# Optimization experiments

Hardware: AMD Instinct MI355X
Metric: run time of the kernel (lower is better)

Reference implementation:

```python
import jax, jax.numpy as jnp
import numpy as np

L, B, S, D, H, FF, V = 4, 2, 1024, 768, 12, 3072, 50257
HD = D // H  # 64
EPS = 1e-5


def _ln(x, w, b):
    m = jnp.mean(x, axis=-1, keepdims=True)
    v = jnp.mean(jnp.square(x - m), axis=-1, keepdims=True)
    return (x - m) * jax.lax.rsqrt(v + EPS) * w + b


def setup_inputs() -> dict:
    key = jax.random.key(0)
    ks = jax.random.split(key, 8)
    std = 0.02
    inp = {
        'input_ids': jax.random.randint(ks[0], (B, S), 0, V),
        'tok_emb': jax.random.normal(ks[1], (V, D), jnp.float32) * std,
        'pos_emb': jax.random.normal(ks[2], (S, D), jnp.float32) * std,
        'ln1_w': jnp.ones((L, D), jnp.float32),
        'ln1_b': jnp.zeros((L, D), jnp.float32),
        'qkv_w': jax.random.normal(ks[3], (L, 3 * D, D), jnp.float32) * std,
        'qkv_b': jnp.zeros((L, 3 * D), jnp.float32),
        'out_w': jax.random.normal(ks[4], (L, D, D), jnp.float32) * std,
        'out_b': jnp.zeros((L, D), jnp.float32),
        'ln2_w': jnp.ones((L, D), jnp.float32),
        'ln2_b': jnp.zeros((L, D), jnp.float32),
        'fc1_w': jax.random.normal(ks[5], (L, FF, D), jnp.float32) * std,
        'fc1_b': jnp.zeros((L, FF), jnp.float32),
        'fc2_w': jax.random.normal(ks[6], (L, D, FF), jnp.float32) * std,
        'fc2_b': jnp.zeros((L, D), jnp.float32),
        'lnf_w': jnp.ones((D,), jnp.float32),
        'lnf_b': jnp.zeros((D,), jnp.float32),
    }
    return inp


def _gpt_forward(input_ids, tok_emb, pos_emb, ln1_w, ln1_b, qkv_w, qkv_b,
                 out_w, out_b, ln2_w, ln2_b, fc1_w, fc1_b, fc2_w, fc2_b,
                 lnf_w, lnf_b):
    x = tok_emb[input_ids] + pos_emb[None, :S, :]  # [B,S,D]
    causal = jnp.tril(jnp.ones((S, S), bool))  # [S,S]
    scale = 1.0 / np.sqrt(HD)
    for l in range(L):
        # --- attention ---
        h = _ln(x, ln1_w[l], ln1_b[l])
        qkv = h @ qkv_w[l].T + qkv_b[l]  # [B,S,3D]
        qkv = qkv.reshape(B, S, 3, H, HD).transpose(2, 0, 3, 1, 4)
        q, k, v = qkv[0], qkv[1], qkv[2]  # [B,H,S,HD]
        scores = jnp.einsum('bhqd,bhkd->bhqk', q, k) * scale
        scores = jnp.where(causal, scores, -jnp.inf)
        w = jax.nn.softmax(scores, axis=-1)
        a = jnp.einsum('bhqk,bhkd->bhqd', w, v)  # [B,H,S,HD]
        a = a.transpose(0, 2, 1, 3).reshape(B, S, D)
        x = x + a @ out_w[l].T + out_b[l]
        # --- ffn ---
        h = _ln(x, ln2_w[l], ln2_b[l])
        h = jax.nn.gelu(h @ fc1_w[l].T + fc1_b[l], approximate=False)
        x = x + h @ fc2_w[l].T + fc2_b[l]
    x = _ln(x, lnf_w, lnf_b)
    logits = x @ tok_emb.T  # tied lm_head, no bias
    return logits


def reference(input_ids, tok_emb, pos_emb, ln1_w, ln1_b, qkv_w, qkv_b,
              out_w, out_b, ln2_w, ln2_b, fc1_w, fc1_b, fc2_w, fc2_b,
              lnf_w, lnf_b):
    return _gpt_forward(input_ids, tok_emb, pos_emb, ln1_w, ln1_b, qkv_w,
                        qkv_b, out_w, out_b, ln2_w, ln2_b, fc1_w, fc1_b,
                        fc2_w, fc2_b, lnf_w, lnf_b)
```

## Files before the change

### kernel.cpp

```cpp
#include <hip/hip_runtime.h>
#include <cstdint>
#include <cstddef>

#define D_MODEL 768
#define NHEAD   12
#define SEQ     1024
#define NTOK    2048
#define FFDIM   3072
#define NLAYER  4
#define VOCAB   50257
#define QKVD    2304

typedef float f32x4 __attribute__((ext_vector_type(4)));
typedef __bf16 bf16x8 __attribute__((ext_vector_type(8)));

__device__ __forceinline__ unsigned short f2bf(float f) {
  unsigned int u = __float_as_uint(f);
  return (unsigned short)((u + 0x7FFFu + ((u >> 16) & 1u)) >> 16);
}

__global__ __launch_bounds__(256) void k_cvt(const float* __restrict__ in,
                                             unsigned short* __restrict__ out, int n8) {
  int i = blockIdx.x * 256 + threadIdx.x;
  if (i >= n8) return;
  const float4* p = (const float4*)in;
  float4 a = p[2 * i], b = p[2 * i + 1];
  union { unsigned short u[8]; uint4 v; } r;
  r.u[0] = f2bf(a.x); r.u[1] = f2bf(a.y); r.u[2] = f2bf(a.z); r.u[3] = f2bf(a.w);
  r.u[4] = f2bf(b.x); r.u[5] = f2bf(b.y); r.u[6] = f2bf(b.z); r.u[7] = f2bf(b.w);
  ((uint4*)out)[i] = r.v;
}

__global__ __launch_bounds__(256) void k_embed(const int* __restrict__ ids,
                                               const float* __restrict__ tok,
                                               const float* __restrict__ pos,
                                               float* __restrict__ x) {
  int gid = blockIdx.x * 256 + threadIdx.x;
  int t = gid / 192, f = gid - t * 192;
  int id = ids[t];
  float4 a = ((const float4*)tok)[(size_t)id * 192 + f];
  float4 b = ((const float4*)pos)[(size_t)(t & (SEQ - 1)) * 192 + f];
  float4 o; o.x = a.x + b.x; o.y = a.y + b.y; o.z = a.z + b.z; o.w = a.w + b.w;
  ((float4*)x)[gid] = o;
}

__global__ __launch_bounds__(256) void k_ln(const float* __restrict__ x,
                                            const float* __restrict__ w,
                                            const float* __restrict__ b,
                                            unsigned short* __restrict__ out) {
  __shared__ float red[256];
  int row = blockIdx.x, tid = threadIdx.x;
  const float* xr = x + (size_t)row * D_MODEL;
  float v0 = xr[tid], v1 = xr[tid + 256], v2 = xr[tid + 512];
  red[tid] = v0 + v1 + v2;
  __syncthreads();
  for (int o = 128; o > 0; o >>= 1) { if (tid < o) red[tid] += red[tid + o]; __syncthreads(); }
  float mean = red[0] * (1.0f / 768.0f);
  __syncthreads();
  float d0 = v0 - mean, d1 = v1 - mean, d2 = v2 - mean;
  red[tid] = d0 * d0 + d1 * d1 + d2 * d2;
  __syncthreads();
  for (int o = 128; o > 0; o >>= 1) { if (tid < o) red[tid] += red[tid + o]; __syncthreads(); }
  float rstd = rsqrtf(red[0] * (1.0f / 768.0f) + 1e-5f);
  unsigned short* orow = out + (size_t)row * D_MODEL;
  orow[tid]       = f2bf(d0 * rstd * w[tid]       + b[tid]);
  orow[tid + 256] = f2bf(d1 * rstd * w[tid + 256] + b[tid + 256]);
  orow[tid + 512] = f2bf(d2 * rstd * w[tid + 512] + b[tid + 512]);
}

__global__ __launch_bounds__(64) void k_attn(const unsigned short* __restrict__ qkv,
                                             unsigned short* __restrict__ attO) {
  int bid = blockIdx.x;
  int qt = (SEQ / 16 - 1) - (bid & 63);
  int h = (bid >> 6) % NHEAD;
  int b = bid / (64 * NHEAD);
  int lane = threadIdx.x;
  int fr = lane & 15, fq = lane >> 4;
  int qb = qt * 16;

  size_t rowQ = (size_t)(b * SEQ + qb + fr) * QKVD + h * 64;
  bf16x8 bq0 = *(const bf16x8*)(qkv + rowQ + fq * 8);
  bf16x8 bq1 = *(const bf16x8*)(qkv + rowQ + 32 + fq * 8);

  float m = -1e30f, ll = 0.0f;
  f32x4 o[4] = {};
  int nkt = (qt >> 1) + 1;
  size_t kvrow0 = (size_t)(b * SEQ) * QKVD;

  for (int kt = 0; kt < nkt; ++kt) {
    int kvb = kt * 32;
    bool diag = (kt == nkt - 1);
    float p[2][4];
    float tm = -1e30f;
    #pragma unroll
    for (int t = 0; t < 2; ++t) {
      size_t rowK = kvrow0 + (size_t)(kvb + t * 16 + fr) * QKVD + D_MODEL + h * 64;
      bf16x8 ak0 = *(const bf16x8*)(qkv + rowK + fq * 8);
      bf16x8 ak1 = *(const bf16x8*)(qkv + rowK + 32 + fq * 8);
      f32x4 st = {};
      st = __builtin_amdgcn_mfma_f32_16x16x32_bf16(ak0, bq0, st, 0, 0, 0);
      st = __builtin_amdgcn_mfma_f32_16x16x32_bf16(ak1, bq1, st, 0, 0, 0);
      #pragma unroll
      for (int j = 0; j < 4; ++j) {
        float s = st[j] * 0.125f;
        if (diag && (kvb + t * 16 + fq * 4 + j > qb + fr)) s = -1e30f;
        p[t][j] = s;
        tm = fmaxf(tm, s);
      }
    }
    tm = fmaxf(tm, __shfl_xor(tm, 16));
    tm = fmaxf(tm, __shfl_xor(tm, 32));
    float mnew = fmaxf(m, tm);
    float corr = __expf(m - mnew);
    float psum = 0.0f;
    #pragma unroll
    for (int t = 0; t < 2; ++t)
      #pragma unroll
      for (int j = 0; j < 4; ++j) { float e = __expf(p[t][j] - mnew); p[t][j] = e; psum += e; }
    psum += __shfl_xor(psum, 16);
    psum += __shfl_xor(psum, 32);
    ll = ll * corr + psum;
    m = mnew;
    #pragma unroll
    for (int dg = 0; dg < 4; ++dg) {
      o[dg][0] *= corr; o[dg][1] *= corr; o[dg][2] *= corr; o[dg][3] *= corr;
    }
    unsigned int lo0 = (unsigned)f2bf(p[0][0]) | ((unsigned)f2bf(p[0][1]) << 16);
    unsigned int hi0 = (unsigned)f2bf(p[0][2]) | ((unsigned)f2bf(p[0][3]) << 16);
    unsigned int lo1 = (unsigned)f2bf(p[1][0]) | ((unsigned)f2bf(p[1][1]) << 16);
    unsigned int hi1 = (unsigned)f2bf(p[1][2]) | ((unsigned)f2bf(p[1][3]) << 16);
    int sA = fr + 16 * ((fq & 1) * 2);
    int sB = sA + 16;
    unsigned int w0a = __shfl(lo0, sA), w0b = __shfl(lo1, sA);
    unsigned int w1a = __shfl(hi0, sA), w1b = __shfl(hi1, sA);
    unsigned int w2a = __shfl(lo0, sB), w2b = __shfl(lo1, sB);
    unsigned int w3a = __shfl(hi0, sB), w3b = __shfl(hi1, sB);
    bool t1 = (fq >> 1) != 0;
    uint4 pw;
    pw.x = t1 ? w0b : w0a;
    pw.y = t1 ? w1b : w1a;
    pw.z = t1 ? w2b : w2a;
    pw.w = t1 ? w3b : w3a;
    bf16x8 pb = __builtin_bit_cast(bf16x8, pw);
    size_t vcol = kvrow0 + 2 * D_MODEL + h * 64 + fr;
    #pragma unroll
    for (int dg = 0; dg < 4; ++dg) {
      union { unsigned short u[8]; bf16x8 v; } va;
      #pragma unroll
      for (int j = 0; j < 8; ++j)
        va.u[j] = qkv[vcol + (size_t)(kvb + fq * 8 + j) * QKVD + dg * 16];
      o[dg] = __builtin_amdgcn_mfma_f32_16x16x32_bf16(va.v, pb, o[dg], 0, 0, 0);
    }
  }
  float inv = 1.0f / ll;
  size_t obase = (size_t)(b * SEQ + qb + fr) * D_MODEL + h * 64;
  #pragma unroll
  for (int dg = 0; dg < 4; ++dg)
    #pragma unroll
    for (int j = 0; j < 4; ++j)
      attO[obase + dg * 16 + fq * 4 + j] = f2bf(o[dg][j] * inv);
}

template<int HAS_BIAS, int DO_GELU, int HAS_RES, int OUT_BF16>
__global__ __launch_bounds__(256) void k_gemm(const unsigned short* __restrict__ A,
                                              const unsigned short* __restrict__ W,
                                              const float* __restrict__ bias,
                                              const float* __restrict__ res,
                                              void* __restrict__ Cout,
                                              int N, int K) {
  __shared__ __align__(1024) unsigned short As[128 * 64];
  __shared__ __align__(1024) unsigned short Ws[128 * 64];
  int tid = threadIdx.x, lane = tid & 63, wv = tid >> 6;
  int fr = lane & 15, fq = lane >> 4;
  int wm = wv >> 1, wn = wv & 1;

  int cpx = gridDim.x >> 3;
  int id = (blockIdx.x & 7) * cpx + (blockIdx.x >> 3);
  int bm = (id & 15) * 128;
  int bn = (id >> 4) * 128;

  const unsigned short* pA[4];
  const unsigned short* pW[4];
  unsigned short* ldsA[4];
  unsigned short* ldsW[4];
  #pragma unroll
  for (int i = 0; i < 4; ++i) {
    int c = wv * 4 + i;
    int r = c * 8 + (lane >> 3);
    int up = (lane & 7) ^ (r & 7);
    pA[i] = A + (size_t)(bm + r) * K + up * 8;
    int wr = bn + r; if (wr > N - 1) wr = N - 1;
    pW[i] = W + (size_t)wr * K + up * 8;
    ldsA[i] = &As[c * 512];
    ldsW[i] = &Ws[c * 512];
  }

  const unsigned short* aB = As + (wm * 64 + fr) * 64;
  const unsigned short* wB = Ws + (wn * 64 + fr) * 64;
  int sz = fr & 7;
  int u0 = (fq ^ sz) * 8;
  int u1 = ((4 + fq) ^ sz) * 8;

  f32x4 acc[4][4] = {};

  for (int k0 = 0; k0 < K; k0 += 64) {
    #pragma unroll
    for (int i = 0; i < 4; ++i) {
      __builtin_amdgcn_global_load_lds(
          (const __attribute__((address_space(1))) unsigned int*)(pA[i] + k0),
          (__attribute__((address_space(3))) unsigned int*)ldsA[i], 16, 0, 0);
      __builtin_amdgcn_global_load_lds(
          (const __attribute__((address_space(1))) unsigned int*)(pW[i] + k0),
          (__attribute__((address_space(3))) unsigned int*)ldsW[i], 16, 0, 0);
    }
    __syncthreads();

    bf16x8 af[4][2], bf[4][2];
    #pragma unroll
    for (int mm = 0; mm < 4; ++mm) {
      af[mm][0] = *(const bf16x8*)(aB + mm * 1024 + u0);
      af[mm][1] = *(const bf16x8*)(aB + mm * 1024 + u1);
    }
    #pragma unroll
    for (int nn = 0; nn < 4; ++nn) {
      bf[nn][0] = *(const bf16x8*)(wB + nn * 1024 + u0);
      bf[nn][1] = *(const bf16x8*)(wB + nn * 1024 + u1);
    }
    #pragma unroll
    for (int mm = 0; mm < 4; ++mm)
      #pragma unroll
      for (int nn = 0; nn < 4; ++nn) {
        acc[mm][nn] = __builtin_amdgcn_mfma_f32_16x16x32_bf16(af[mm][0], bf[nn][0], acc[mm][nn], 0, 0, 0);
        acc[mm][nn] = __builtin_amdgcn_mfma_f32_16x16x32_bf16(af[mm][1], bf[nn][1], acc[mm][nn], 0, 0, 0);
      }
    __syncthreads();
  }

  #pragma unroll
  for (int nn = 0; nn < 4; ++nn) {
    int col = bn + wn * 64 + nn * 16 + fr;
    if (col >= N) continue;
    float bv = HAS_BIAS ? bias[col] : 0.0f;
    #pragma unroll
    for (int mm = 0; mm < 4; ++mm) {
      #pragma unroll
      for (int j = 0; j < 4; ++j) {
        int row = bm + wm * 64 + mm * 16 + fq * 4 + j;
        size_t idx = (size_t)row * N + col;
        float v = acc[mm][nn][j] + bv;
        if (DO_GELU) v = 0.5f * v * (1.0f + erff(v * 0.70710678118f));
        if (HAS_RES) v += res[idx];
        if (OUT_BF16) ((unsigned short*)Cout)[idx] = f2bf(v);
        else          ((float*)Cout)[idx] = v;
      }
    }
  }
}

extern "C" void kernel_launch(void* const* d_in, const int* in_sizes, int n_in,
                              void* d_out, int out_size, void* d_ws, size_t ws_size,
                              hipStream_t stream) {
  const int*   ids    = (const int*)d_in[0];
  const float* tok    = (const float*)d_in[1];
  const float* pos    = (const float*)d_in[2];
  const float* ln1_w  = (const float*)d_in[3];
  const float* ln1_b  = (const float*)d_in[4];
  const float* qkv_w  = (const float*)d_in[5];
  const float* qkv_b  = (const float*)d_in[6];
  const float* out_w  = (const float*)d_in[7];
  const float* out_b  = (const float*)d_in[8];
  const float* ln2_w  = (const float*)d_in[9];
  const float* ln2_b  = (const float*)d_in[10];
  const float* fc1_w  = (const float*)d_in[11];
  const float* fc1_b  = (const float*)d_in[12];
  const float* fc2_w  = (const float*)d_in[13];
  const float* fc2_b  = (const float*)d_in[14];
  const float* lnf_w  = (const float*)d_in[15];
  const float* lnf_b  = (const float*)d_in[16];

  char* ws = (char*)d_ws;
  float*          x    = (float*)(ws);
  unsigned short* qkvb = (unsigned short*)(ws + 6291456);
  unsigned short* h    = (unsigned short*)(ws + 15728640);
  unsigned short* attO = (unsigned short*)(ws + 18874368);
  unsigned short* gbuf = (unsigned short*)(ws + 22020096);
  unsigned short* wq   = (unsigned short*)(ws + 34603008);
  unsigned short* wo   = (unsigned short*)(ws + 48758784);
  unsigned short* w1   = (unsigned short*)(ws + 53477376);
  unsigned short* w2   = (unsigned short*)(ws + 72351744);
  unsigned short* wtok = (unsigned short*)(ws + 91226112);
  float* logits = (float*)d_out;

  {
    int n8;
    n8 = NLAYER * QKVD * D_MODEL / 8;
    k_cvt<<<(n8 + 255) / 256, 256, 0, stream>>>(qkv_w, wq, n8);
    n8 = NLAYER * D_MODEL * D_MODEL / 8;
    k_cvt<<<(n8 + 255) / 256, 256, 0, stream>>>(out_w, wo, n8);
    n8 = NLAYER * FFDIM * D_MODEL / 8;
    k_cvt<<<(n8 + 255) / 256, 256, 0, stream>>>(fc1_w, w1, n8);
    k_cvt<<<(n8 + 255) / 256, 256, 0, stream>>>(fc2_w, w2, n8);
    n8 = VOCAB * D_MODEL / 8;
    k_cvt<<<(n8 + 255) / 256, 256, 0, stream>>>(tok, wtok, n8);
  }

  k_embed<<<NTOK * 192 / 256, 256, 0, stream>>>(ids, tok, pos, x);

  for (int l = 0; l < NLAYER; ++l) {
    k_ln<<<NTOK, 256, 0, stream>>>(x, ln1_w + l * D_MODEL, ln1_b + l * D_MODEL, h);
    k_gemm<1, 0, 0, 1><<<16 * (QKVD / 128), 256, 0, stream>>>(
        h, wq + (size_t)l * QKVD * D_MODEL, qkv_b + l * QKVD, nullptr, qkvb, QKVD, D_MODEL);
    k_attn<<<2 * NHEAD * (SEQ / 16), 64, 0, stream>>>(qkvb, attO);
    k_gemm<1, 0, 1, 0><<<16 * (D_MODEL / 128), 256, 0, stream>>>(
        attO, wo + (size_t)l * D_MODEL * D_MODEL, out_b + l * D_MODEL, x, x, D_MODEL, D_MODEL);
    k_ln<<<NTOK, 256, 0, stream>>>(x, ln2_w + l * D_MODEL, ln2_b + l * D_MODEL, h);
    k_gemm<1, 1, 0, 1><<<16 * (FFDIM / 128), 256, 0, stream>>>(
        h, w1 + (size_t)l * FFDIM * D_MODEL, fc1_b + l * FFDIM, nullptr, gbuf, FFDIM, D_MODEL);
    k_gemm<1, 0, 1, 0><<<16 * (D_MODEL / 128), 256, 0, stream>>>(
        gbuf, w2 + (size_t)l * D_MODEL * FFDIM, fc2_b + l * D_MODEL, x, x, D_MODEL, FFDIM);
  }

  k_ln<<<NTOK, 256, 0, stream>>>(x, lnf_w, lnf_b, h);
  k_gemm<0, 0, 0, 0><<<16 * ((VOCAB + 127) / 128), 256, 0, stream>>>(
      h, wtok, nullptr, nullptr, logits, VOCAB, D_MODEL);
}
```

Baseline: 1.149 ms.

## Add 256x256-tile triple-buffered GEMM for the LM head projection

Adds a dedicated 512-thread GEMM kernel for the vocabulary projection. It uses 256x256 output tiles, direct global-to-LDS loads into a three-stage swizzled buffer, split MFMA phases with priority hints, and a grouped block order for L2 reuse. The goal is to raise data reuse and overlap loads with compute on the largest GEMM, which writes about 100M fp32 logits. In exchange it uses more LDS and registers per block, and the last N tile is partial and wastes work.

Result: slower. 1.215 ms (+5.7%).

```diff
diff --git a/kernel.cpp b/kernel.cpp
--- a/kernel.cpp
+++ b/kernel.cpp
@@ -257,6 +257,116 @@
   }
 }
 
+#define STAGE_A256(tt, bsel) do { \
+  __builtin_amdgcn_global_load_lds( \
+      (const __attribute__((address_space(1))) unsigned int*)(srcA0 + (size_t)(tt) * 32), \
+      (__attribute__((address_space(3))) unsigned int*)(&As3[bsel][ldsc0]), 16, 0, 0); \
+  __builtin_amdgcn_global_load_lds( \
+      (const __attribute__((address_space(1))) unsigned int*)(srcA1 + (size_t)(tt) * 32), \
+      (__attribute__((address_space(3))) unsigned int*)(&As3[bsel][ldsc1]), 16, 0, 0); } while (0)
+#define STAGE_W256(tt, bsel) do { \
+  __builtin_amdgcn_global_load_lds( \
+      (const __attribute__((address_space(1))) unsigned int*)(srcW0 + (size_t)(tt) * 32), \
+      (__attribute__((address_space(3))) unsigned int*)(&Ws3[bsel][ldsc0]), 16, 0, 0); \
+  __builtin_amdgcn_global_load_lds( \
+      (const __attribute__((address_space(1))) unsigned int*)(srcW1 + (size_t)(tt) * 32), \
+      (__attribute__((address_space(3))) unsigned int*)(&Ws3[bsel][ldsc1]), 16, 0, 0); } while (0)
+
+__global__ __launch_bounds__(512, 2) void k_gemm256(const unsigned short* __restrict__ A,
+                                                    const unsigned short* __restrict__ W,
+                                                    float* __restrict__ C,
+                                                    int N, int K) {
+  __shared__ __align__(1024) unsigned short As3[3][8192];
+  __shared__ __align__(1024) unsigned short Ws3[3][8192];
+  const int tid = threadIdx.x, lane = tid & 63, wv = tid >> 6;
+  const int fr = lane & 15, fq = lane >> 4;
+  const int wm = wv >> 2, wn = wv & 3;
+
+  int q = gridDim.x >> 3;
+  int id = ((int)blockIdx.x & 7) * q + ((int)blockIdx.x >> 3);
+  int bm = (id & 7) * 256;
+  int bn = (id >> 3) * 256;
+
+  const int su = (lane & 3) ^ ((lane >> 3) & 3);
+  const int c0 = wv * 2, c1 = wv * 2 + 1;
+  const int r0 = c0 * 16 + (lane >> 2), r1 = c1 * 16 + (lane >> 2);
+  const unsigned short* srcA0 = A + (size_t)(bm + r0) * K + su * 8;
+  const unsigned short* srcA1 = A + (size_t)(bm + r1) * K + su * 8;
+  int wr0 = bn + r0; if (wr0 > N - 1) wr0 = N - 1;
+  int wr1 = bn + r1; if (wr1 > N - 1) wr1 = N - 1;
+  const unsigned short* srcW0 = W + (size_t)wr0 * K + su * 8;
+  const unsigned short* srcW1 = W + (size_t)wr1 * K + su * 8;
+  const int ldsc0 = c0 * 512, ldsc1 = c1 * 512;
+
+  const int rsw = (fq ^ ((fr >> 1) & 3)) * 8;
+  const int aoff = (wm * 128 + fr) * 32 + rsw;
+  const int woff = (wn * 64 + fr) * 32 + rsw;
+
+  f32x4 acc[8][4] = {};
+  const int NT = K >> 5;
+
+  STAGE_A256(0, 0); STAGE_W256(0, 0);
+  STAGE_A256(1, 1); STAGE_W256(1, 1);
+  asm volatile("s_waitcnt vmcnt(4)" ::: "memory");
+  __builtin_amdgcn_s_barrier();
+
+  int bsel = 0;
+  for (int t = 0; t < NT; ++t) {
+    const unsigned short* ab = &As3[bsel][0] + aoff;
+    const unsigned short* wb = &Ws3[bsel][0] + woff;
+    int nb = bsel + 2; if (nb >= 3) nb -= 3;
+    bf16x8 af[4], bf[4];
+    #pragma unroll
+    for (int m = 0; m < 4; ++m) af[m] = *(const bf16x8*)(ab + m * 512);
+    #pragma unroll
+    for (int n = 0; n < 4; ++n) bf[n] = *(const bf16x8*)(wb + n * 512);
+    if (t + 2 < NT) STAGE_A256(t + 2, nb);
+    __builtin_amdgcn_s_barrier();
+    asm volatile("s_waitcnt lgkmcnt(0)" ::: "memory");
+    __builtin_amdgcn_s_setprio(1);
+    #pragma unroll
+    for (int m = 0; m < 4; ++m)
+      #pragma unroll
+      for (int n = 0; n < 4; ++n)
+        acc[m][n] = __builtin_amdgcn_mfma_f32_16x16x32_bf16(af[m], bf[n], acc[m][n], 0, 0, 0);
+    __builtin_amdgcn_s_setprio(0);
+    #pragma unroll
+    for (int m = 0; m < 4; ++m) af[m] = *(const bf16x8*)(ab + (m + 4) * 512);
+    if (t + 2 < NT) {
+      STAGE_W256(t + 2, nb);
+      asm volatile("s_waitcnt vmcnt(4)" ::: "memory");
+    } else if (t + 1 < NT) {
+      asm volatile("s_waitcnt vmcnt(0)" ::: "memory");
+    }
+    __builtin_amdgcn_s_barrier();
+    asm volatile("s_waitcnt lgkmcnt(0)" ::: "memory");
+    __builtin_amdgcn_s_setprio(1);
+    #pragma unroll
+    for (int m = 0; m < 4; ++m)
+      #pragma unroll
+      for (int n = 0; n < 4; ++n)
+        acc[m + 4][n] = __builtin_amdgcn_mfma_f32_16x16x32_bf16(af[m], bf[n], acc[m + 4][n], 0, 0, 0);
+    __builtin_amdgcn_s_setprio(0);
+    __builtin_amdgcn_s_barrier();
+    bsel += 1; if (bsel == 3) bsel = 0;
+  }
+
+  #pragma unroll
+  for (int n = 0; n < 4; ++n) {
+    int col = bn + wn * 64 + n * 16 + fr;
+    if (col >= N) continue;
+    #pragma unroll
+    for (int m = 0; m < 8; ++m) {
+      int row = bm + wm * 128 + m * 16 + fq * 4;
+      float* cp = C + (size_t)row * N + col;
+      cp[0] = acc[m][n][0];
+      cp[(size_t)N] = acc[m][n][1];
+      cp[(size_t)2 * N] = acc[m][n][2];
+      cp[(size_t)3 * N] = acc[m][n][3];
+    }
+  }
+}
+
 extern "C" void kernel_launch(void* const* d_in, const int* in_sizes, int n_in,
                               void* d_out, int out_size, void* d_ws, size_t ws_size,
                               hipStream_t stream) {
@@ -321,6 +431,5 @@
   }
 
   k_ln<<<NTOK, 256, 0, stream>>>(x, lnf_w, lnf_b, h);
-  k_gemm<0, 0, 0, 0><<<16 * ((VOCAB + 127) / 128), 256, 0, stream>>>(
-      h, wtok, nullptr, nullptr, logits, VOCAB, D_MODEL);
-}
+  k_gemm256<<<8 * ((VOCAB + 255) / 256), 512, 0, stream>>>(h, wtok, logits, VOCAB, D_MODEL);
+}
```

## Pre-transpose V for attention and vectorize GEMM epilogue via swapped MFMA operands

Applied to the files above, without the earlier changes.

Adds a kernel that transposes the V slice of the QKV buffer into a per-head [D,S] layout, reusing the LN scratch buffer. The attention kernel can then load V fragments with single 16-byte loads instead of eight strided scalar loads. The GEMM swaps MFMA operand order so each lane holds four consecutive output columns, which allows vectorized bias, residual and output accesses. This costs an extra launch and transpose traffic per layer, and the logits output with odd N falls back to scalar stores.

Result: slower. 1.370 ms (+19.2%).

```diff
diff --git a/kernel.cpp b/kernel.cpp
--- a/kernel.cpp
+++ b/kernel.cpp
@@ -68,7 +68,31 @@
   orow[tid + 512] = f2bf(d2 * rstd * w[tid + 512] + b[tid + 512]);
 }
 
+__global__ __launch_bounds__(256) void k_vt(const unsigned short* __restrict__ qkv,
+                                            unsigned short* __restrict__ vt) {
+  __shared__ unsigned short t[64][80];
+  int bid = blockIdx.x;
+  int st = bid & 15, h = (bid >> 4) % NHEAD, b = bid / (16 * NHEAD);
+  int tid = threadIdx.x;
+  int r = tid >> 2, cq = (tid & 3) * 16;
+  const unsigned short* src =
+      qkv + (size_t)(b * SEQ + st * 64 + r) * QKVD + 2 * D_MODEL + h * 64 + cq;
+  *(uint4*)&t[r][cq] = *(const uint4*)src;
+  *(uint4*)&t[r][cq + 8] = *(const uint4*)(src + 8);
+  __syncthreads();
+  int d = r, j0 = cq;
+  unsigned short* dst = vt + ((size_t)(b * D_MODEL) + h * 64 + d) * SEQ + st * 64 + j0;
+  union { unsigned short u[8]; uint4 v; } o0, o1;
+  #pragma unroll
+  for (int jj = 0; jj < 8; ++jj) o0.u[jj] = t[j0 + jj][d];
+  #pragma unroll
+  for (int jj = 0; jj < 8; ++jj) o1.u[jj] = t[j0 + 8 + jj][d];
+  *(uint4*)dst = o0.v;
+  *(uint4*)(dst + 8) = o1.v;
+}
+
 __global__ __launch_bounds__(64) void k_attn(const unsigned short* __restrict__ qkv,
+                                             const unsigned short* __restrict__ vt,
                                              unsigned short* __restrict__ attO) {
   int bid = blockIdx.x;
   int qt = (SEQ / 16 - 1) - (bid & 63);
@@ -86,6 +110,7 @@
   f32x4 o[4] = {};
   int nkt = (qt >> 1) + 1;
   size_t kvrow0 = (size_t)(b * SEQ) * QKVD;
+  const unsigned short* vbase0 = vt + ((size_t)(b * D_MODEL) + h * 64 + fr) * SEQ;
 
   for (int kt = 0; kt < nkt; ++kt) {
     int kvb = kt * 32;
@@ -142,14 +167,11 @@
     pw.z = t1 ? w2b : w2a;
     pw.w = t1 ? w3b : w3a;
     bf16x8 pb = __builtin_bit_cast(bf16x8, pw);
-    size_t vcol = kvrow0 + 2 * D_MODEL + h * 64 + fr;
+    const unsigned short* vp = vbase0 + kvb + fq * 8;
     #pragma unroll
     for (int dg = 0; dg < 4; ++dg) {
-      union { unsigned short u[8]; bf16x8 v; } va;
-      #pragma unroll
-      for (int j = 0; j < 8; ++j)
-        va.u[j] = qkv[vcol + (size_t)(kvb + fq * 8 + j) * QKVD + dg * 16];
-      o[dg] = __builtin_amdgcn_mfma_f32_16x16x32_bf16(va.v, pb, o[dg], 0, 0, 0);
+      bf16x8 va = *(const bf16x8*)(vp + (size_t)dg * 16 * SEQ);
+      o[dg] = __builtin_amdgcn_mfma_f32_16x16x32_bf16(va, pb, o[dg], 0, 0, 0);
     }
   }
   float inv = 1.0f / ll;
@@ -230,28 +252,50 @@
     for (int mm = 0; mm < 4; ++mm)
       #pragma unroll
       for (int nn = 0; nn < 4; ++nn) {
-        acc[mm][nn] = __builtin_amdgcn_mfma_f32_16x16x32_bf16(af[mm][0], bf[nn][0], acc[mm][nn], 0, 0, 0);
-        acc[mm][nn] = __builtin_amdgcn_mfma_f32_16x16x32_bf16(af[mm][1], bf[nn][1], acc[mm][nn], 0, 0, 0);
+        acc[mm][nn] = __builtin_amdgcn_mfma_f32_16x16x32_bf16(bf[nn][0], af[mm][0], acc[mm][nn], 0, 0, 0);
+        acc[mm][nn] = __builtin_amdgcn_mfma_f32_16x16x32_bf16(bf[nn][1], af[mm][1], acc[mm][nn], 0, 0, 0);
       }
     __syncthreads();
   }
 
   #pragma unroll
-  for (int nn = 0; nn < 4; ++nn) {
-    int col = bn + wn * 64 + nn * 16 + fr;
-    if (col >= N) continue;
-    float bv = HAS_BIAS ? bias[col] : 0.0f;
-    #pragma unroll
-    for (int mm = 0; mm < 4; ++mm) {
-      #pragma unroll
-      for (int j = 0; j < 4; ++j) {
-        int row = bm + wm * 64 + mm * 16 + fq * 4 + j;
-        size_t idx = (size_t)row * N + col;
-        float v = acc[mm][nn][j] + bv;
-        if (DO_GELU) v = 0.5f * v * (1.0f + erff(v * 0.70710678118f));
-        if (HAS_RES) v += res[idx];
-        if (OUT_BF16) ((unsigned short*)Cout)[idx] = f2bf(v);
-        else          ((float*)Cout)[idx] = v;
+  for (int mm = 0; mm < 4; ++mm) {
+    int row = bm + wm * 64 + mm * 16 + fr;
+    #pragma unroll
+    for (int nn = 0; nn < 4; ++nn) {
+      int col = bn + wn * 64 + nn * 16 + fq * 4;
+      if (col >= N) continue;
+      f32x4 v = acc[mm][nn];
+      if (HAS_BIAS) {
+        float4 bv = *(const float4*)(bias + col);
+        v[0] += bv.x; v[1] += bv.y; v[2] += bv.z; v[3] += bv.w;
+      }
+      if (DO_GELU) {
+        #pragma unroll
+        for (int j = 0; j < 4; ++j)
+          v[j] = 0.5f * v[j] * (1.0f + erff(v[j] * 0.70710678118f));
+      }
+      size_t idx = (size_t)row * N + col;
+      if (HAS_RES) {
+        float4 rv = *(const float4*)(res + idx);
+        v[0] += rv.x; v[1] += rv.y; v[2] += rv.z; v[3] += rv.w;
+      }
+      if (OUT_BF16) {
+        union { unsigned short u[4]; unsigned long long q; } ob;
+        ob.u[0] = f2bf(v[0]); ob.u[1] = f2bf(v[1]);
+        ob.u[2] = f2bf(v[2]); ob.u[3] = f2bf(v[3]);
+        *(unsigned long long*)((unsigned short*)Cout + idx) = ob.q;
+      } else {
+        float* cp = (float*)Cout + idx;
+        if ((N & 3) == 0) {
+          *(f32x4*)cp = v;
+        } else {
+          int rem = N - col;
+          if (rem > 0) cp[0] = v[0];
+          if (rem > 1) cp[1] = v[1];
+          if (rem > 2) cp[2] = v[2];
+          if (rem > 3) cp[3] = v[3];
+        }
       }
     }
   }
@@ -310,7 +354,8 @@
     k_ln<<<NTOK, 256, 0, stream>>>(x, ln1_w + l * D_MODEL, ln1_b + l * D_MODEL, h);
     k_gemm<1, 0, 0, 1><<<16 * (QKVD / 128), 256, 0, stream>>>(
         h, wq + (size_t)l * QKVD * D_MODEL, qkv_b + l * QKVD, nullptr, qkvb, QKVD, D_MODEL);
-    k_attn<<<2 * NHEAD * (SEQ / 16), 64, 0, stream>>>(qkvb, attO);
+    k_vt<<<2 * NHEAD * 16, 256, 0, stream>>>(qkvb, h);
+    k_attn<<<2 * NHEAD * (SEQ / 16), 64, 0, stream>>>(qkvb, h, attO);
     k_gemm<1, 0, 1, 0><<<16 * (D_MODEL / 128), 256, 0, stream>>>(
         attO, wo + (size_t)l * D_MODEL * D_MODEL, out_b + l * D_MODEL, x, x, D_MODEL, D_MODEL);
     k_ln<<<NTOK, 256, 0, stream>>>(x, ln2_w + l * D_MODEL, ln2_b + l * D_MODEL, h);
```

## Pre-transpose V per head so attention loads V with vector reads

Applied to the files above, without the earlier changes.

Adds a kernel that transposes each head's V slice into a [B, D, S] buffer, reusing the LN scratch buffer h, which is free at that point. The attention kernel then loads V fragments as contiguous 16-byte vectors instead of eight strided 2-byte gathers per MFMA operand. This removes uncoalesced scalar loads from the inner attention loop. The cost is an extra kernel launch and one extra read and write of V per layer.

Measured after the change: 1.202 ms. 1.05x slower.

```diff
diff --git a/kernel.cpp b/kernel.cpp
--- a/kernel.cpp
+++ b/kernel.cpp
@@ -68,7 +68,31 @@
   orow[tid + 512] = f2bf(d2 * rstd * w[tid + 512] + b[tid + 512]);
 }
 
+__global__ __launch_bounds__(256) void k_vt(const unsigned short* __restrict__ qkv,
+                                            unsigned short* __restrict__ vt) {
+  __shared__ unsigned short t[64][80];
+  int bid = blockIdx.x;
+  int st = bid & 15, h = (bid >> 4) % NHEAD, b = bid / (16 * NHEAD);
+  int tid = threadIdx.x;
+  int r = tid >> 2, cq = (tid & 3) * 16;
+  const unsigned short* src =
+      qkv + (size_t)(b * SEQ + st * 64 + r) * QKVD + 2 * D_MODEL + h * 64 + cq;
+  *(uint4*)&t[r][cq] = *(const uint4*)src;
+  *(uint4*)&t[r][cq + 8] = *(const uint4*)(src + 8);
+  __syncthreads();
+  int d = r, j0 = cq;
+  unsigned short* dst = vt + ((size_t)(b * D_MODEL) + h * 64 + d) * SEQ + st * 64 + j0;
+  union { unsigned short u[8]; uint4 v; } o0, o1;
+  #pragma unroll
+  for (int jj = 0; jj < 8; ++jj) o0.u[jj] = t[j0 + jj][d];
+  #pragma unroll
+  for (int jj = 0; jj < 8; ++jj) o1.u[jj] = t[j0 + 8 + jj][d];
+  *(uint4*)dst = o0.v;
+  *(uint4*)(dst + 8) = o1.v;
+}
+
 __global__ __launch_bounds__(64) void k_attn(const unsigned short* __restrict__ qkv,
+                                             const unsigned short* __restrict__ vt,
                                              unsigned short* __restrict__ attO) {
   int bid = blockIdx.x;
   int qt = (SEQ / 16 - 1) - (bid & 63);
@@ -86,6 +110,7 @@
   f32x4 o[4] = {};
   int nkt = (qt >> 1) + 1;
   size_t kvrow0 = (size_t)(b * SEQ) * QKVD;
+  const unsigned short* vbase0 = vt + ((size_t)(b * D_MODEL) + h * 64 + fr) * SEQ;
 
   for (int kt = 0; kt < nkt; ++kt) {
     int kvb = kt * 32;
@@ -142,14 +167,11 @@
     pw.z = t1 ? w2b : w2a;
     pw.w = t1 ? w3b : w3a;
     bf16x8 pb = __builtin_bit_cast(bf16x8, pw);
-    size_t vcol = kvrow0 + 2 * D_MODEL + h * 64 + fr;
+    const unsigned short* vp = vbase0 + kvb + fq * 8;
     #pragma unroll
     for (int dg = 0; dg < 4; ++dg) {
-      union { unsigned short u[8]; bf16x8 v; } va;
-      #pragma unroll
-      for (int j = 0; j < 8; ++j)
-        va.u[j] = qkv[vcol + (size_t)(kvb + fq * 8 + j) * QKVD + dg * 16];
-      o[dg] = __builtin_amdgcn_mfma_f32_16x16x32_bf16(va.v, pb, o[dg], 0, 0, 0);
+      bf16x8 va = *(const bf16x8*)(vp + (size_t)dg * 16 * SEQ);
+      o[dg] = __builtin_amdgcn_mfma_f32_16x16x32_bf16(va, pb, o[dg], 0, 0, 0);
     }
   }
   float inv = 1.0f / ll;
@@ -310,7 +332,8 @@
     k_ln<<<NTOK, 256, 0, stream>>>(x, ln1_w + l * D_MODEL, ln1_b + l * D_MODEL, h);
     k_gemm<1, 0, 0, 1><<<16 * (QKVD / 128), 256, 0, stream>>>(
         h, wq + (size_t)l * QKVD * D_MODEL, qkv_b + l * QKVD, nullptr, qkvb, QKVD, D_MODEL);
-    k_attn<<<2 * NHEAD * (SEQ / 16), 64, 0, stream>>>(qkvb, attO);
+    k_vt<<<2 * NHEAD * 16, 256, 0, stream>>>(qkvb, h);
+    k_attn<<<2 * NHEAD * (SEQ / 16), 64, 0, stream>>>(qkvb, h, attO);
     k_gemm<1, 0, 1, 0><<<16 * (D_MODEL / 128), 256, 0, stream>>>(
         attO, wo + (size_t)l * D_MODEL * D_MODEL, out_b + l * D_MODEL, x, x, D_MODEL, D_MODEL);
     k_ln<<<NTOK, 256, 0, stream>>>(x, ln2_w + l * D_MODEL, ln2_b + l * D_MODEL, h);
```
